# Kernel optimization log

Measured on AMD Instinct MI355X. Metric: run time of the kernel, lower is better.

The kernel has to match this reference:

```python
import jax, jax.numpy as jnp
import numpy as np

B, LQ, LK, D, H = 4, 1024, 1024, 512, 8
HD = D // H
NEG_SLOPE = 0.2


def setup_inputs() -> dict:
    key = jax.random.key(0)
    k1, k2, k3, k4, k5 = jax.random.split(key, 5)
    query = jax.random.normal(k1, (B, LQ, D), dtype=jnp.float32)
    key_t = jax.random.normal(k2, (B, LK, D), dtype=jnp.float32)
    value = jax.random.normal(k3, (B, LK, D), dtype=jnp.float32)
    mask = jnp.ones((B, LQ, LK), dtype=jnp.int32)
    # xavier-uniform-like init for params
    limW = float(np.sqrt(6.0 / (D + D)))
    W = jax.random.uniform(k4, (D, D), minval=-limW, maxval=limW, dtype=jnp.float32)
    lima = float(np.sqrt(6.0 / (H + 2 * HD)))
    a = jax.random.uniform(k5, (1, H, 2 * HD), minval=-lima, maxval=lima, dtype=jnp.float32)
    return {"query": query, "key": key_t, "value": value, "mask": mask, "W": W, "a": a}


def reference(query, key, value, mask, W, a):
    b, lq, d = query.shape
    lk = key.shape[1]
    h = a.shape[1]
    hd = a.shape[2] // 2
    # shared linear projection (nn.Linear: x @ W.T)
    Q = (query @ W.T).reshape(b, lq, h, hd)
    K = (key @ W.T).reshape(b, lk, h, hd)
    V = (value @ W.T).reshape(b, lk, h, hd)
    # a^T [Q || K] = a_q . Q + a_k . K  (avoids the (b,lq,lk,h,2hd) concat)
    a_q = a[0, :, :hd]  # (h, hd)
    a_k = a[0, :, hd:]
    sq = jnp.einsum('bqhd,hd->bhq', Q, a_q)
    sk = jnp.einsum('bkhd,hd->bhk', K, a_k)
    scores = sq[:, :, :, None] + sk[:, :, None, :]  # (b, h, lq, lk)
    scores = jnp.where(scores >= 0, scores, NEG_SLOPE * scores)  # LeakyReLU
    scores = jnp.where(mask[:, None, :, :] == 0, -jnp.inf, scores)
    attn = jax.nn.softmax(scores, axis=-1)
    attn = jnp.where(jnp.isnan(attn), 0.0, attn)  # fully-masked rows -> 0
    out = jnp.einsum('bhqk,bkhd->bqhd', attn, V).reshape(b, lq, d)
    return out
```

## Files before the change

kernel.cpp:

```cpp
#include <hip/hip_runtime.h>
#include <hip/hip_bf16.h>

#define NEG_SLOPE 0.2f

constexpr int B = 4, LQ = 1024, LK = 1024, D = 512, H = 8, HD = 64;

typedef __attribute__((ext_vector_type(8))) short bf16x8;
typedef __attribute__((ext_vector_type(4))) float f32x4;

static __device__ __forceinline__ ushort f2bf(float x) {
  return __builtin_bit_cast(ushort, __float2bfloat16(x));
}
static __device__ __forceinline__ float bf2f(ushort u) {
  return __bfloat162float(__builtin_bit_cast(__hip_bfloat16, u));
}

__global__ void prep_wqwk(const float* __restrict__ W, const float* __restrict__ a,
                          float* __restrict__ wq, float* __restrict__ wk) {
  int tid = blockIdx.x * blockDim.x + threadIdx.x;
  int h = tid >> 9, j = tid & 511;
  const float* aq = a + h * 2 * HD;
  const float* ak = aq + HD;
  float accq = 0.f, acck = 0.f;
#pragma unroll 8
  for (int d = 0; d < HD; ++d) {
    float w = W[(size_t)(h * HD + d) * D + j];
    accq = fmaf(aq[d], w, accq);
    acck = fmaf(ak[d], w, acck);
  }
  wq[tid] = accq;
  wk[tid] = acck;
}

__global__ __launch_bounds__(256) void sqsk_kernel(
    const float* __restrict__ query, const float* __restrict__ key,
    const float* __restrict__ wq, const float* __restrict__ wk,
    float* __restrict__ sq, float* __restrict__ sk) {
  int gw = (blockIdx.x * blockDim.x + threadIdx.x) >> 6;
  int lane = threadIdx.x & 63;
  bool isK = gw >= B * LQ;
  int row = isK ? gw - B * LQ : gw;
  const float* x = (isK ? key : query) + (size_t)row * D + lane * 8;
  const float* wbase = isK ? wk : wq;
  float4 x0 = *(const float4*)x;
  float4 x1 = *(const float4*)(x + 4);
  float acc[H];
#pragma unroll
  for (int h = 0; h < H; ++h) {
    const float* w = wbase + h * D + lane * 8;
    float4 w0 = *(const float4*)w;
    float4 w1 = *(const float4*)(w + 4);
    acc[h] = x0.x * w0.x + x0.y * w0.y + x0.z * w0.z + x0.w * w0.w +
             x1.x * w1.x + x1.y * w1.y + x1.z * w1.z + x1.w * w1.w;
  }
#pragma unroll
  for (int off = 32; off > 0; off >>= 1) {
#pragma unroll
    for (int h = 0; h < H; ++h) acc[h] += __shfl_xor(acc[h], off, 64);
  }
  if (lane == 0) {
    int b = row >> 10, pos = row & 1023;
    float* dst = isK ? sk : sq;
#pragma unroll
    for (int h = 0; h < H; ++h) dst[((size_t)(b * H + h) << 10) + pos] = acc[h];
  }
}

__global__ __launch_bounds__(256) void cvt_split(
    const float* __restrict__ value, const float* __restrict__ W,
    ushort* __restrict__ val_hi, ushort* __restrict__ val_lo,
    ushort* __restrict__ w_hi, ushort* __restrict__ w_lo) {
  constexpr int VAL4 = B * LK * D / 4;
  constexpr int W4 = D * D / 4;
  int idx = blockIdx.x * 256 + threadIdx.x;
  if (idx >= VAL4 + W4) return;
  const float* src;
  ushort *dhi, *dlo;
  int off;
  if (idx < VAL4) { src = value; dhi = val_hi; dlo = val_lo; off = idx; }
  else           { src = W;     dhi = w_hi;   dlo = w_lo;   off = idx - VAL4; }
  float4 x = ((const float4*)src)[off];
  float xs[4] = {x.x, x.y, x.z, x.w};
  ushort hs[4], ls[4];
#pragma unroll
  for (int i = 0; i < 4; ++i) {
    hs[i] = f2bf(xs[i]);
    ls[i] = f2bf(xs[i] - bf2f(hs[i]));
  }
  ((ushort4*)dhi)[off] = make_ushort4(hs[0], hs[1], hs[2], hs[3]);
  ((ushort4*)dlo)[off] = make_ushort4(ls[0], ls[1], ls[2], ls[3]);
}

__global__ __launch_bounds__(256) void maskbits_kernel(const int* __restrict__ mask,
                                                       unsigned int* __restrict__ mbits) {
  int gw = (blockIdx.x * 256 + threadIdx.x) >> 6;
  int lane = threadIdx.x & 63;
#pragma unroll 4
  for (int it = 0; it < 64; ++it) {
    int wv = gw + it * 1024;
    int mv = mask[(size_t)wv * 64 + lane];
    unsigned long long bal = __ballot(mv != 0);
    if (lane == 0) *(unsigned long long*)&mbits[wv * 2] = bal;
  }
}

__global__ __launch_bounds__(256) void vproj_mfma(
    const ushort* __restrict__ val_hi, const ushort* __restrict__ val_lo,
    const ushort* __restrict__ w_hi, const ushort* __restrict__ w_lo,
    ushort* __restrict__ vt_hi, ushort* __restrict__ vt_lo) {
  __shared__ ushort as_hi[64][40], as_lo[64][40], bs_hi[64][40], bs_lo[64][40];
  int r0 = blockIdx.x * 64, c0 = blockIdx.y * 64;
  int tid = threadIdx.x, w = tid >> 6, lane = tid & 63;
  int wr = w >> 1, wc = w & 1;
  int ln15 = lane & 15, kg = lane >> 4;
  f32x4 acc[2][2] = {};
  int srow = tid >> 2, sch = (tid & 3) * 8;
  for (int k0 = 0; k0 < D; k0 += 32) {
    __syncthreads();
    *(float4*)&as_hi[srow][sch] = *(const float4*)&val_hi[(size_t)(r0 + srow) * D + k0 + sch];
    *(float4*)&as_lo[srow][sch] = *(const float4*)&val_lo[(size_t)(r0 + srow) * D + k0 + sch];
    *(float4*)&bs_hi[srow][sch] = *(const float4*)&w_hi[(size_t)(c0 + srow) * D + k0 + sch];
    *(float4*)&bs_lo[srow][sch] = *(const float4*)&w_lo[(size_t)(c0 + srow) * D + k0 + sch];
    __syncthreads();
    bf16x8 ah[2], al[2], bh[2], bl[2];
#pragma unroll
    for (int f = 0; f < 2; ++f) {
      int ra = wr * 32 + f * 16 + ln15;
      ah[f] = *(const bf16x8*)&as_hi[ra][kg * 8];
      al[f] = *(const bf16x8*)&as_lo[ra][kg * 8];
      int rb = wc * 32 + f * 16 + ln15;
      bh[f] = *(const bf16x8*)&bs_hi[rb][kg * 8];
      bl[f] = *(const bf16x8*)&bs_lo[rb][kg * 8];
    }
#pragma unroll
    for (int fm = 0; fm < 2; ++fm)
#pragma unroll
      for (int fn = 0; fn < 2; ++fn) {
        acc[fm][fn] = __builtin_amdgcn_mfma_f32_16x16x32_bf16(ah[fm], bh[fn], acc[fm][fn], 0, 0, 0);
        acc[fm][fn] = __builtin_amdgcn_mfma_f32_16x16x32_bf16(al[fm], bh[fn], acc[fm][fn], 0, 0, 0);
        acc[fm][fn] = __builtin_amdgcn_mfma_f32_16x16x32_bf16(ah[fm], bl[fn], acc[fm][fn], 0, 0, 0);
      }
  }
#pragma unroll
  for (int fm = 0; fm < 2; ++fm)
#pragma unroll
    for (int fn = 0; fn < 2; ++fn) {
      int rrow = r0 + wr * 32 + fm * 16 + (lane >> 4) * 4;
      int col = c0 + wc * 32 + fn * 16 + ln15;
      int b = rrow >> 10, k = rrow & 1023;
      int h = col >> 6, dd = col & 63;
      size_t base = ((size_t)((b * H + h) * HD + dd) << 10) + k;
      ushort hv[4], lv[4];
#pragma unroll
      for (int r = 0; r < 4; ++r) {
        float v = acc[fm][fn][r];
        hv[r] = f2bf(v);
        lv[r] = f2bf(v - bf2f(hv[r]));
      }
      *(ushort4*)&vt_hi[base] = make_ushort4(hv[0], hv[1], hv[2], hv[3]);
      *(ushort4*)&vt_lo[base] = make_ushort4(lv[0], lv[1], lv[2], lv[3]);
    }
}

__global__ __launch_bounds__(256) void attn_mfma(
    const float* __restrict__ sq, const float* __restrict__ sk,
    const unsigned int* __restrict__ mbits,
    const ushort* __restrict__ vt_hi, const ushort* __restrict__ vt_lo,
    float* __restrict__ out) {
  __shared__ float sks[LK];
  __shared__ ushort vhs[64][136], vls[64][136];
  __shared__ float linv_s[4][16];
  int bh = blockIdx.x, b = bh >> 3, h = bh & 7;
  int q0 = blockIdx.y * 64;
  int tid = threadIdx.x, w = tid >> 6, lane = tid & 63;
  int ln15 = lane & 15, kg = lane >> 4;
  int qs = q0 + w * 16 + ln15;
#pragma unroll
  for (int i = 0; i < 4; ++i) sks[i * 256 + tid] = sk[((size_t)bh << 10) + i * 256 + tid];
  float sqv = sq[((size_t)bh << 10) + qs];
  const unsigned int* mrow = mbits + ((size_t)(b << 10) + qs) * (LK / 32);
  const ushort* vhbase = vt_hi + (((size_t)bh * HD) << 10);
  const ushort* vlbase = vt_lo + (((size_t)bh * HD) << 10);
  f32x4 acc[4] = {};
  float lsum = 0.f;
  for (int tile = 0; tile < 8; ++tile) {
    int k0 = tile * 128;
    __syncthreads();
#pragma unroll
    for (int c = 0; c < 4; ++c) {
      int id = c * 256 + tid;
      int d = id >> 4, ch = id & 15;
      *(float4*)&vhs[d][ch * 8] = *(const float4*)&vhbase[((size_t)d << 10) + k0 + ch * 8];
      *(float4*)&vls[d][ch * 8] = *(const float4*)&vlbase[((size_t)d << 10) + k0 + ch * 8];
    }
    __syncthreads();
#pragma unroll
    for (int ks = 0; ks < 4; ++ks) {
      int kb = k0 + ks * 32;
      unsigned int wb = mrow[kb >> 5];
      float skv[8];
      *(float4*)&skv[0] = *(const float4*)&sks[kb + kg * 8];
      *(float4*)&skv[4] = *(const float4*)&sks[kb + kg * 8 + 4];
      bf16x8 phi, plo;
#pragma unroll
      for (int i = 0; i < 8; ++i) {
        float s = sqv + skv[i];
        float f = fmaxf(s, NEG_SLOPE * s);
        float p = ((wb >> (kg * 8 + i)) & 1u) ? __expf(f - 8.0f) : 0.f;
        lsum += p;
        ushort hb = f2bf(p);
        phi[i] = (short)hb;
        plo[i] = (short)f2bf(p - bf2f(hb));
      }
#pragma unroll
      for (int df = 0; df < 4; ++df) {
        int drow = df * 16 + ln15;
        bf16x8 bhv = *(const bf16x8*)&vhs[drow][ks * 32 + kg * 8];
        bf16x8 blv = *(const bf16x8*)&vls[drow][ks * 32 + kg * 8];
        acc[df] = __builtin_amdgcn_mfma_f32_16x16x32_bf16(phi, bhv, acc[df], 0, 0, 0);
        acc[df] = __builtin_amdgcn_mfma_f32_16x16x32_bf16(plo, bhv, acc[df], 0, 0, 0);
        acc[df] = __builtin_amdgcn_mfma_f32_16x16x32_bf16(phi, blv, acc[df], 0, 0, 0);
      }
    }
  }
  lsum += __shfl_xor(lsum, 16, 64);
  lsum += __shfl_xor(lsum, 32, 64);
  if (lane < 16) linv_s[w][ln15] = (lsum > 0.f) ? 1.f / lsum : 0.f;
  __syncthreads();
#pragma unroll
  for (int df = 0; df < 4; ++df) {
#pragma unroll
    for (int r = 0; r < 4; ++r) {
      int qrow = q0 + w * 16 + (lane >> 4) * 4 + r;
      float inv = linv_s[w][(lane >> 4) * 4 + r];
      int col = h * HD + df * 16 + ln15;
      out[((size_t)(b << 10) + qrow) * D + col] = acc[df][r] * inv;
    }
  }
}

extern "C" void kernel_launch(void* const* d_in, const int* in_sizes, int n_in,
                              void* d_out, int out_size, void* d_ws, size_t ws_size,
                              hipStream_t stream) {
  const float* query = (const float*)d_in[0];
  const float* key   = (const float*)d_in[1];
  const float* value = (const float*)d_in[2];
  const int*   mask  = (const int*)d_in[3];
  const float* W     = (const float*)d_in[4];
  const float* a     = (const float*)d_in[5];
  float* out = (float*)d_out;

  char* ws = (char*)d_ws;
  float* wq = (float*)ws;                    ws += 4096 * 4;
  float* wk = (float*)ws;                    ws += 4096 * 4;
  float* sq = (float*)ws;                    ws += 32768 * 4;
  float* sk = (float*)ws;                    ws += 32768 * 4;
  ushort* val_hi = (ushort*)ws;              ws += (size_t)B * LK * D * 2;
  ushort* val_lo = (ushort*)ws;              ws += (size_t)B * LK * D * 2;
  ushort* w_hi = (ushort*)ws;                ws += (size_t)D * D * 2;
  ushort* w_lo = (ushort*)ws;                ws += (size_t)D * D * 2;
  ushort* vt_hi = (ushort*)ws;               ws += (size_t)B * H * HD * LK * 2;
  ushort* vt_lo = (ushort*)ws;               ws += (size_t)B * H * HD * LK * 2;
  unsigned int* mbits = (unsigned int*)ws;   ws += (size_t)B * LQ * LK / 32 * 4;

  prep_wqwk<<<dim3(16), dim3(256), 0, stream>>>(W, a, wq, wk);
  cvt_split<<<dim3((B * LK * D / 4 + D * D / 4 + 255) / 256), dim3(256), 0, stream>>>(
      value, W, val_hi, val_lo, w_hi, w_lo);
  maskbits_kernel<<<dim3(256), dim3(256), 0, stream>>>(mask, mbits);
  sqsk_kernel<<<dim3(2 * B * LQ / 4), dim3(256), 0, stream>>>(query, key, wq, wk, sq, sk);
  vproj_mfma<<<dim3(B * LK / 64, D / 64), dim3(256), 0, stream>>>(
      val_hi, val_lo, w_hi, w_lo, vt_hi, vt_lo);
  attn_mfma<<<dim3(B * H, LQ / 64), dim3(256), 0, stream>>>(
      sq, sk, mbits, vt_hi, vt_lo, out);
}
```

Before: 156.3 us.

## Fuse auxiliary prep kernels and register-prefetch tiles in projection and attention

Three separate preprocessing kernels (value/W bf16 split, mask bit packing, sq/sk score projection) are merged into one launch, selected by block-index ranges. This removes launch gaps and lets the independent work overlap. The V-projection GEMM now uses a 64-wide K tile and prefetches the next tile into registers while the MFMAs run on the current one. The attention kernel gets the same register prefetch of V tiles. The cost is more live registers (which may lower occupancy) and more LDS in the projection kernel.

```diff
diff --git a/kernel.cpp b/kernel.cpp
--- a/kernel.cpp
+++ b/kernel.cpp
@@ -32,75 +32,73 @@
   wk[tid] = acck;
 }
 
-__global__ __launch_bounds__(256) void sqsk_kernel(
+__global__ __launch_bounds__(256) void fused_aux(
     const float* __restrict__ query, const float* __restrict__ key,
+    const float* __restrict__ value, const int* __restrict__ mask,
+    const float* __restrict__ W,
     const float* __restrict__ wq, const float* __restrict__ wk,
+    ushort* __restrict__ val_hi, ushort* __restrict__ val_lo,
+    ushort* __restrict__ w_hi, ushort* __restrict__ w_lo,
+    unsigned int* __restrict__ mbits,
     float* __restrict__ sq, float* __restrict__ sk) {
-  int gw = (blockIdx.x * blockDim.x + threadIdx.x) >> 6;
-  int lane = threadIdx.x & 63;
-  bool isK = gw >= B * LQ;
-  int row = isK ? gw - B * LQ : gw;
-  const float* x = (isK ? key : query) + (size_t)row * D + lane * 8;
-  const float* wbase = isK ? wk : wq;
-  float4 x0 = *(const float4*)x;
-  float4 x1 = *(const float4*)(x + 4);
-  float acc[H];
-#pragma unroll
-  for (int h = 0; h < H; ++h) {
-    const float* w = wbase + h * D + lane * 8;
-    float4 w0 = *(const float4*)w;
-    float4 w1 = *(const float4*)(w + 4);
-    acc[h] = x0.x * w0.x + x0.y * w0.y + x0.z * w0.z + x0.w * w0.w +
-             x1.x * w1.x + x1.y * w1.y + x1.z * w1.z + x1.w * w1.w;
-  }
-#pragma unroll
-  for (int off = 32; off > 0; off >>= 1) {
-#pragma unroll
-    for (int h = 0; h < H; ++h) acc[h] += __shfl_xor(acc[h], off, 64);
-  }
-  if (lane == 0) {
-    int b = row >> 10, pos = row & 1023;
-    float* dst = isK ? sk : sq;
-#pragma unroll
-    for (int h = 0; h < H; ++h) dst[((size_t)(b * H + h) << 10) + pos] = acc[h];
-  }
-}
-
-__global__ __launch_bounds__(256) void cvt_split(
-    const float* __restrict__ value, const float* __restrict__ W,
-    ushort* __restrict__ val_hi, ushort* __restrict__ val_lo,
-    ushort* __restrict__ w_hi, ushort* __restrict__ w_lo) {
-  constexpr int VAL4 = B * LK * D / 4;
-  constexpr int W4 = D * D / 4;
-  int idx = blockIdx.x * 256 + threadIdx.x;
-  if (idx >= VAL4 + W4) return;
-  const float* src;
-  ushort *dhi, *dlo;
-  int off;
-  if (idx < VAL4) { src = value; dhi = val_hi; dlo = val_lo; off = idx; }
-  else           { src = W;     dhi = w_hi;   dlo = w_lo;   off = idx - VAL4; }
-  float4 x = ((const float4*)src)[off];
-  float xs[4] = {x.x, x.y, x.z, x.w};
-  ushort hs[4], ls[4];
-#pragma unroll
-  for (int i = 0; i < 4; ++i) {
-    hs[i] = f2bf(xs[i]);
-    ls[i] = f2bf(xs[i] - bf2f(hs[i]));
-  }
-  ((ushort4*)dhi)[off] = make_ushort4(hs[0], hs[1], hs[2], hs[3]);
-  ((ushort4*)dlo)[off] = make_ushort4(ls[0], ls[1], ls[2], ls[3]);
-}
-
-__global__ __launch_bounds__(256) void maskbits_kernel(const int* __restrict__ mask,
-                                                       unsigned int* __restrict__ mbits) {
-  int gw = (blockIdx.x * 256 + threadIdx.x) >> 6;
-  int lane = threadIdx.x & 63;
+  int blk = blockIdx.x, tid = threadIdx.x;
+  if (blk < 2304) {
+    constexpr int VAL4 = B * LK * D / 4;
+    int idx = blk * 256 + tid;
+    const float* src;
+    ushort *dhi, *dlo;
+    int off;
+    if (idx < VAL4) { src = value; dhi = val_hi; dlo = val_lo; off = idx; }
+    else           { src = W;     dhi = w_hi;   dlo = w_lo;   off = idx - VAL4; }
+    float4 x = ((const float4*)src)[off];
+    float xs[4] = {x.x, x.y, x.z, x.w};
+    ushort hs[4], ls[4];
+#pragma unroll
+    for (int i = 0; i < 4; ++i) {
+      hs[i] = f2bf(xs[i]);
+      ls[i] = f2bf(xs[i] - bf2f(hs[i]));
+    }
+    ((ushort4*)dhi)[off] = make_ushort4(hs[0], hs[1], hs[2], hs[3]);
+    ((ushort4*)dlo)[off] = make_ushort4(ls[0], ls[1], ls[2], ls[3]);
+  } else if (blk < 2560) {
+    int gw = ((blk - 2304) * 256 + tid) >> 6;
+    int lane = tid & 63;
 #pragma unroll 4
-  for (int it = 0; it < 64; ++it) {
-    int wv = gw + it * 1024;
-    int mv = mask[(size_t)wv * 64 + lane];
-    unsigned long long bal = __ballot(mv != 0);
-    if (lane == 0) *(unsigned long long*)&mbits[wv * 2] = bal;
+    for (int it = 0; it < 64; ++it) {
+      int wv = gw + it * 1024;
+      int mv = mask[(size_t)wv * 64 + lane];
+      unsigned long long bal = __ballot(mv != 0);
+      if (lane == 0) *(unsigned long long*)&mbits[wv * 2] = bal;
+    }
+  } else {
+    int gw = ((blk - 2560) * 256 + tid) >> 6;
+    int lane = tid & 63;
+    bool isK = gw >= B * LQ;
+    int row = isK ? gw - B * LQ : gw;
+    const float* x = (isK ? key : query) + (size_t)row * D + lane * 8;
+    const float* wbase = isK ? wk : wq;
+    float4 x0 = *(const float4*)x;
+    float4 x1 = *(const float4*)(x + 4);
+    float acc[H];
+#pragma unroll
+    for (int h = 0; h < H; ++h) {
+      const float* w = wbase + h * D + lane * 8;
+      float4 w0 = *(const float4*)w;
+      float4 w1 = *(const float4*)(w + 4);
+      acc[h] = x0.x * w0.x + x0.y * w0.y + x0.z * w0.z + x0.w * w0.w +
+               x1.x * w1.x + x1.y * w1.y + x1.z * w1.z + x1.w * w1.w;
+    }
+#pragma unroll
+    for (int off = 32; off > 0; off >>= 1) {
+#pragma unroll
+      for (int h = 0; h < H; ++h) acc[h] += __shfl_xor(acc[h], off, 64);
+    }
+    if (lane == 0) {
+      int b = row >> 10, pos = row & 1023;
+      float* dst = isK ? sk : sq;
+#pragma unroll
+      for (int h = 0; h < H; ++h) dst[((size_t)(b * H + h) << 10) + pos] = acc[h];
+    }
   }
 }
 
@@ -108,39 +106,72 @@
     const ushort* __restrict__ val_hi, const ushort* __restrict__ val_lo,
     const ushort* __restrict__ w_hi, const ushort* __restrict__ w_lo,
     ushort* __restrict__ vt_hi, ushort* __restrict__ vt_lo) {
-  __shared__ ushort as_hi[64][40], as_lo[64][40], bs_hi[64][40], bs_lo[64][40];
+  __shared__ ushort as_hi[64][72], as_lo[64][72], bs_hi[64][72], bs_lo[64][72];
   int r0 = blockIdx.x * 64, c0 = blockIdx.y * 64;
   int tid = threadIdx.x, w = tid >> 6, lane = tid & 63;
   int wr = w >> 1, wc = w & 1;
   int ln15 = lane & 15, kg = lane >> 4;
   f32x4 acc[2][2] = {};
-  int srow = tid >> 2, sch = (tid & 3) * 8;
-  for (int k0 = 0; k0 < D; k0 += 32) {
+  int srow = tid >> 2, scol = (tid & 3) * 16;
+  const size_t arow = (size_t)(r0 + srow) * D;
+  const size_t brow = (size_t)(c0 + srow) * D;
+  float4 ra0, ra1, rb0, rb1, rc0, rc1, rd0, rd1;
+#define VLOAD(k0)                                                      \
+  do {                                                                 \
+    ra0 = *(const float4*)&val_hi[arow + (k0) + scol];                 \
+    ra1 = *(const float4*)&val_hi[arow + (k0) + scol + 8];             \
+    rb0 = *(const float4*)&val_lo[arow + (k0) + scol];                 \
+    rb1 = *(const float4*)&val_lo[arow + (k0) + scol + 8];             \
+    rc0 = *(const float4*)&w_hi[brow + (k0) + scol];                   \
+    rc1 = *(const float4*)&w_hi[brow + (k0) + scol + 8];               \
+    rd0 = *(const float4*)&w_lo[brow + (k0) + scol];                   \
+    rd1 = *(const float4*)&w_lo[brow + (k0) + scol + 8];               \
+  } while (0)
+#define VSTORE()                                                       \
+  do {                                                                 \
+    *(float4*)&as_hi[srow][scol] = ra0;                                \
+    *(float4*)&as_hi[srow][scol + 8] = ra1;                            \
+    *(float4*)&as_lo[srow][scol] = rb0;                                \
+    *(float4*)&as_lo[srow][scol + 8] = rb1;                            \
+    *(float4*)&bs_hi[srow][scol] = rc0;                                \
+    *(float4*)&bs_hi[srow][scol + 8] = rc1;                            \
+    *(float4*)&bs_lo[srow][scol] = rd0;                                \
+    *(float4*)&bs_lo[srow][scol + 8] = rd1;                            \
+  } while (0)
+  VLOAD(0);
+  VSTORE();
+  __syncthreads();
+  for (int kt = 0; kt < 8; ++kt) {
+    if (kt < 7) VLOAD((kt + 1) * 64);
+#pragma unroll
+    for (int ks2 = 0; ks2 < 2; ++ks2) {
+      bf16x8 ah[2], al[2], bh[2], bl[2];
+#pragma unroll
+      for (int f = 0; f < 2; ++f) {
+        int ra = wr * 32 + f * 16 + ln15;
+        ah[f] = *(const bf16x8*)&as_hi[ra][ks2 * 32 + kg * 8];
+        al[f] = *(const bf16x8*)&as_lo[ra][ks2 * 32 + kg * 8];
+        int rb = wc * 32 + f * 16 + ln15;
+        bh[f] = *(const bf16x8*)&bs_hi[rb][ks2 * 32 + kg * 8];
+        bl[f] = *(const bf16x8*)&bs_lo[rb][ks2 * 32 + kg * 8];
+      }
+#pragma unroll
+      for (int fm = 0; fm < 2; ++fm)
+#pragma unroll
+        for (int fn = 0; fn < 2; ++fn) {
+          acc[fm][fn] = __builtin_amdgcn_mfma_f32_16x16x32_bf16(ah[fm], bh[fn], acc[fm][fn], 0, 0, 0);
+          acc[fm][fn] = __builtin_amdgcn_mfma_f32_16x16x32_bf16(al[fm], bh[fn], acc[fm][fn], 0, 0, 0);
+          acc[fm][fn] = __builtin_amdgcn_mfma_f32_16x16x32_bf16(ah[fm], bl[fn], acc[fm][fn], 0, 0, 0);
+        }
+    }
     __syncthreads();
-    *(float4*)&as_hi[srow][sch] = *(const float4*)&val_hi[(size_t)(r0 + srow) * D + k0 + sch];
-    *(float4*)&as_lo[srow][sch] = *(const float4*)&val_lo[(size_t)(r0 + srow) * D + k0 + sch];
-    *(float4*)&bs_hi[srow][sch] = *(const float4*)&w_hi[(size_t)(c0 + srow) * D + k0 + sch];
-    *(float4*)&bs_lo[srow][sch] = *(const float4*)&w_lo[(size_t)(c0 + srow) * D + k0 + sch];
-    __syncthreads();
-    bf16x8 ah[2], al[2], bh[2], bl[2];
-#pragma unroll
-    for (int f = 0; f < 2; ++f) {
-      int ra = wr * 32 + f * 16 + ln15;
-      ah[f] = *(const bf16x8*)&as_hi[ra][kg * 8];
-      al[f] = *(const bf16x8*)&as_lo[ra][kg * 8];
-      int rb = wc * 32 + f * 16 + ln15;
-      bh[f] = *(const bf16x8*)&bs_hi[rb][kg * 8];
-      bl[f] = *(const bf16x8*)&bs_lo[rb][kg * 8];
-    }
-#pragma unroll
-    for (int fm = 0; fm < 2; ++fm)
-#pragma unroll
-      for (int fn = 0; fn < 2; ++fn) {
-        acc[fm][fn] = __builtin_amdgcn_mfma_f32_16x16x32_bf16(ah[fm], bh[fn], acc[fm][fn], 0, 0, 0);
-        acc[fm][fn] = __builtin_amdgcn_mfma_f32_16x16x32_bf16(al[fm], bh[fn], acc[fm][fn], 0, 0, 0);
-        acc[fm][fn] = __builtin_amdgcn_mfma_f32_16x16x32_bf16(ah[fm], bl[fn], acc[fm][fn], 0, 0, 0);
-      }
-  }
+    if (kt < 7) {
+      VSTORE();
+      __syncthreads();
+    }
+  }
+#undef VLOAD
+#undef VSTORE
 #pragma unroll
   for (int fm = 0; fm < 2; ++fm)
 #pragma unroll
@@ -181,22 +212,34 @@
   const unsigned int* mrow = mbits + ((size_t)(b << 10) + qs) * (LK / 32);
   const ushort* vhbase = vt_hi + (((size_t)bh * HD) << 10);
   const ushort* vlbase = vt_lo + (((size_t)bh * HD) << 10);
+  int sdb = tid >> 4, sch = (tid & 15) * 8;
+  float4 rh[4], rl[4];
+#define ALOAD(k0)                                                            \
+  {                                                                          \
+    _Pragma("unroll") for (int c = 0; c < 4; ++c) {                          \
+      int d = c * 16 + sdb;                                                  \
+      rh[c] = *(const float4*)&vhbase[((size_t)d << 10) + (k0) + sch];       \
+      rl[c] = *(const float4*)&vlbase[((size_t)d << 10) + (k0) + sch];       \
+    }                                                                        \
+  }
+#define ASTORE()                                                             \
+  {                                                                          \
+    _Pragma("unroll") for (int c = 0; c < 4; ++c) {                          \
+      int d = c * 16 + sdb;                                                  \
+      *(float4*)&vhs[d][sch] = rh[c];                                        \
+      *(float4*)&vls[d][sch] = rl[c];                                        \
+    }                                                                        \
+  }
+  ALOAD(0);
+  ASTORE();
+  __syncthreads();
   f32x4 acc[4] = {};
   float lsum = 0.f;
   for (int tile = 0; tile < 8; ++tile) {
-    int k0 = tile * 128;
-    __syncthreads();
-#pragma unroll
-    for (int c = 0; c < 4; ++c) {
-      int id = c * 256 + tid;
-      int d = id >> 4, ch = id & 15;
-      *(float4*)&vhs[d][ch * 8] = *(const float4*)&vhbase[((size_t)d << 10) + k0 + ch * 8];
-      *(float4*)&vls[d][ch * 8] = *(const float4*)&vlbase[((size_t)d << 10) + k0 + ch * 8];
-    }
-    __syncthreads();
+    if (tile < 7) ALOAD((tile + 1) * 128);
 #pragma unroll
     for (int ks = 0; ks < 4; ++ks) {
-      int kb = k0 + ks * 32;
+      int kb = tile * 128 + ks * 32;
       unsigned int wb = mrow[kb >> 5];
       float skv[8];
       *(float4*)&skv[0] = *(const float4*)&sks[kb + kg * 8];
@@ -222,7 +265,14 @@
         acc[df] = __builtin_amdgcn_mfma_f32_16x16x32_bf16(phi, blv, acc[df], 0, 0, 0);
       }
     }
-  }
+    __syncthreads();
+    if (tile < 7) {
+      ASTORE();
+      __syncthreads();
+    }
+  }
+#undef ALOAD
+#undef ASTORE
   lsum += __shfl_xor(lsum, 16, 64);
   lsum += __shfl_xor(lsum, 32, 64);
   if (lane < 16) linv_s[w][ln15] = (lsum > 0.f) ? 1.f / lsum : 0.f;
@@ -264,10 +314,9 @@
   unsigned int* mbits = (unsigned int*)ws;   ws += (size_t)B * LQ * LK / 32 * 4;
 
   prep_wqwk<<<dim3(16), dim3(256), 0, stream>>>(W, a, wq, wk);
-  cvt_split<<<dim3((B * LK * D / 4 + D * D / 4 + 255) / 256), dim3(256), 0, stream>>>(
-      value, W, val_hi, val_lo, w_hi, w_lo);
-  maskbits_kernel<<<dim3(256), dim3(256), 0, stream>>>(mask, mbits);
-  sqsk_kernel<<<dim3(2 * B * LQ / 4), dim3(256), 0, stream>>>(query, key, wq, wk, sq, sk);
+  fused_aux<<<dim3(4608), dim3(256), 0, stream>>>(
+      query, key, value, mask, W, wq, wk,
+      val_hi, val_lo, w_hi, w_lo, mbits, sq, sk);
   vproj_mfma<<<dim3(B * LK / 64, D / 64), dim3(256), 0, stream>>>(
       val_hi, val_lo, w_hi, w_lo, vt_hi, vt_lo);
   attn_mfma<<<dim3(B * H, LQ / 64), dim3(256), 0, stream>>>(
```

Result: slower. 184.2 us (+17.9%).
